# Kernel optimization log

Hardware: AMD Instinct MI355X
Metric: run time of the kernel (lower is better)

Reference implementation:

```python
import jax, jax.numpy as jnp
import numpy as np

N = 50000
E = 400000
NF = 320
HID = 320
EPS = 1e-08


def _linear(x, W, b=None):
    y = x @ W.T
    return y if b is None else y + b


def setup_inputs() -> dict:
    key = jax.random.key(0)
    ks = jax.random.split(key, 16)
    s = 0.05
    inp = {
        "h": jax.random.normal(ks[0], (N, NF), jnp.float32),
        "coord": jax.random.normal(ks[1], (N, 3), jnp.float32),
        "edge_index": jax.random.randint(ks[2], (2, E), 0, N, jnp.int32),
        # edge_mlp: Linear(2*NF+1 -> HID), SiLU, Linear(HID -> HID), SiLU
        "W_e1": jax.random.normal(ks[3], (HID, 2 * NF + 1), jnp.float32) * s,
        "b_e1": jnp.zeros((HID,), jnp.float32),
        "W_e2": jax.random.normal(ks[4], (HID, HID), jnp.float32) * s,
        "b_e2": jnp.zeros((HID,), jnp.float32),
        # node_mlp: Linear(HID+NF -> HID), SiLU, Linear(HID -> NF)
        "W_n1": jax.random.normal(ks[5], (HID, HID + NF), jnp.float32) * s,
        "b_n1": jnp.zeros((HID,), jnp.float32),
        "W_n2": jax.random.normal(ks[6], (NF, HID), jnp.float32) * s,
        "b_n2": jnp.zeros((NF,), jnp.float32),
        # coord_mlp: Linear(HID -> HID), SiLU, Linear(HID -> 1, no bias, xavier gain .001)
        "W_c1": jax.random.normal(ks[7], (HID, HID), jnp.float32) * s,
        "b_c1": jnp.zeros((HID,), jnp.float32),
        "W_c2": jax.random.normal(ks[8], (1, HID), jnp.float32) * 0.001,
    }
    return inp


def reference(h, coord, edge_index, W_e1, b_e1, W_e2, b_e2,
              W_n1, b_n1, W_n2, b_n2, W_c1, b_c1, W_c2):
    row, col = edge_index[0], edge_index[1]

    # coord2radial (normalize=True hard-coded in the module)
    coord_diff = coord[row] - coord[col]                      # [E,3]
    radial = jnp.sum(coord_diff ** 2, axis=1, keepdims=True)  # [E,1]
    norm = jax.lax.stop_gradient(jnp.sqrt(radial)) + EPS
    coord_diff = coord_diff / norm

    # edge model: gather endpoint feats, MLP with SiLU
    edge_in = jnp.concatenate([h[row], h[col], radial], axis=1)   # [E, 2*NF+1]
    m = jax.nn.silu(_linear(edge_in, W_e1, b_e1))
    m = jax.nn.silu(_linear(m, W_e2, b_e2))                       # [E, HID]

    # coord model: per-edge scalar weight, scatter-sum to nodes
    w = _linear(jax.nn.silu(_linear(m, W_c1, b_c1)), W_c2)        # [E,1]
    trans = coord_diff * w                                        # [E,3]
    coord_agg = jax.ops.segment_sum(trans, row, num_segments=N)   # [N,3]
    coord_out = coord + coord_agg

    # node model: scatter-sum messages, MLP, residual
    agg = jax.ops.segment_sum(m, row, num_segments=N)             # [N,HID]
    node_in = jnp.concatenate([h, agg], axis=1)                   # [N,HID+NF]
    out = _linear(jax.nn.silu(_linear(node_in, W_n1, b_n1)), W_n2, b_n2)
    h_out = h + out

    return (h_out, coord_out)
```

## Files before the change

### kernel.cpp

```cpp
#include <hip/hip_runtime.h>

#define NN 50000
#define NE 400000
#define NFD 320
#define NB1 196

typedef short bf16x8 __attribute__((ext_vector_type(8)));
typedef float f32x4 __attribute__((ext_vector_type(4)));

#define MFMA16 __builtin_amdgcn_mfma_f32_16x16x32_bf16

__device__ __forceinline__ unsigned short f2bf(float f){
  unsigned int u = __float_as_uint(f);
  u += 0x7fffu + ((u >> 16) & 1u);
  return (unsigned short)(u >> 16);
}
__device__ __forceinline__ unsigned int cvt_pk_bf16(float lo, float hi){
  unsigned int r;
  asm("v_cvt_pk_bf16_f32 %0, %1, %2" : "=v"(r) : "v"(lo), "v"(hi));
  return r;
}
__device__ __forceinline__ float bflo(unsigned int q){ return __uint_as_float(q << 16); }
__device__ __forceinline__ float bfhi(unsigned int q){ return __uint_as_float(q & 0xffff0000u); }
__device__ __forceinline__ float rcp_fast(float x){
  float r;
  asm("v_rcp_f32 %0, %1" : "=v"(r) : "v"(x));
  return r;
}
__device__ __forceinline__ float silu_f(float x){
  return x * rcp_fast(1.f + __expf(-x));
}

__device__ __forceinline__ void pack_w_body(const float* __restrict__ W,
                                            unsigned short* __restrict__ P,
                                            int kstride, int KS, int idx){
  if (idx >= 20 * KS * 64) return;
  int lane = idx & 63;
  int t  = idx >> 6;
  int ks = t % KS;
  int ct = t / KS;
  const float* src = W + (size_t)(ct*16 + (lane & 15)) * kstride + ks*32 + 8*(lane >> 4);
  unsigned int q[4];
  #pragma unroll
  for (int j = 0; j < 4; j++) q[j] = cvt_pk_bf16(src[2*j], src[2*j+1]);
  *(uint4*)(P + (size_t)idx * 8) = make_uint4(q[0], q[1], q[2], q[3]);
}

__device__ __forceinline__ void pack_stack_body(const float* __restrict__ We1,
                                                unsigned short* __restrict__ P, int idx){
  if (idx >= 40 * 10 * 64) return;
  int lane = idx & 63;
  int t  = idx >> 6;
  int ks = t % 10;
  int ct = t / 10;
  int o  = ct*16 + (lane & 15);
  int k  = ks*32 + 8*(lane >> 4);
  const float* src = (o < 320) ? (We1 + (size_t)o * 641 + k)
                               : (We1 + (size_t)(o - 320) * 641 + 320 + k);
  unsigned int q[4];
  #pragma unroll
  for (int j = 0; j < 4; j++) q[j] = cvt_pk_bf16(src[2*j], src[2*j+1]);
  *(uint4*)(P + (size_t)idx * 8) = make_uint4(q[0], q[1], q[2], q[3]);
}

#define PREP_PACK_B 176
#define PREP_CIN_B  293
#define PREP_HIST_B 782
__global__ void __launch_bounds__(512)
prep_k(const float* __restrict__ We2, const float* __restrict__ Wc1,
       const float* __restrict__ Wn1, const float* __restrict__ Wn2,
       const float* __restrict__ We1,
       unsigned short* __restrict__ We2p, unsigned short* __restrict__ Wc1p,
       unsigned short* __restrict__ Wn1p, unsigned short* __restrict__ Wn2p,
       unsigned short* __restrict__ Wsp, float* __restrict__ we1l,
       const float* __restrict__ coord, float* __restrict__ outc,
       const int* __restrict__ ei, int* __restrict__ cnt){
  int b = blockIdx.x;
  int tid = threadIdx.x;
  if (b < PREP_PACK_B){
    int idx = b*512 + tid;
    if (idx < 12800)       pack_w_body(We2, We2p, 320, 10, idx);
    else if (idx < 25600)  pack_w_body(Wc1, Wc1p, 320, 10, idx - 12800);
    else if (idx < 51200)  pack_w_body(Wn1, Wn1p, 640, 20, idx - 25600);
    else if (idx < 64000)  pack_w_body(Wn2, Wn2p, 320, 10, idx - 51200);
    else if (idx < 89600)  pack_stack_body(We1, Wsp, idx - 64000);
    else if (idx < 89920){
      int o = idx - 89600;
      we1l[o] = We1[(size_t)o * 641 + 640];
    }
  } else if (b < PREP_PACK_B + PREP_CIN_B){
    int i = (b - PREP_PACK_B)*512 + tid;
    if (i < NN*3) outc[i] = coord[i];
  } else {
    int e = (b - PREP_PACK_B - PREP_CIN_B)*512 + tid;
    if (e < NE) atomicAdd(&cnt[ei[e]], 1);
  }
}

__global__ void scan1(const int* __restrict__ cnt, int* __restrict__ cur,
                      int* __restrict__ bsum){
  __shared__ int sh[256];
  int tid = threadIdx.x;
  int i = blockIdx.x * 256 + tid;
  int v = (i < NN) ? cnt[i] : 0;
  sh[tid] = v;
  __syncthreads();
  for (int d = 1; d < 256; d <<= 1){
    int u = (tid >= d) ? sh[tid - d] : 0;
    __syncthreads();
    sh[tid] += u;
    __syncthreads();
  }
  if (i < NN) cur[i] = sh[tid] - v;
  if (tid == 255) bsum[blockIdx.x] = sh[255];
}

__global__ void scan2(int* __restrict__ bsum){
  __shared__ int sh[256];
  int tid = threadIdx.x;
  int v = (tid < NB1) ? bsum[tid] : 0;
  sh[tid] = v;
  __syncthreads();
  for (int d = 1; d < 256; d <<= 1){
    int u = (tid >= d) ? sh[tid - d] : 0;
    __syncthreads();
    sh[tid] += u;
    __syncthreads();
  }
  if (tid < NB1) bsum[tid] = sh[tid] - v;
}

__global__ void scan3(int* __restrict__ cur, const int* __restrict__ bsum){
  int i = blockIdx.x * 256 + threadIdx.x;
  if (i < NN) cur[i] += bsum[blockIdx.x];
}

__device__ __forceinline__ void gemm5(const unsigned short* __restrict__ s,
                                      const unsigned short* __restrict__ wp,
                                      int arow0, int arow1, int kl,
                                      int fragbase, int KST, int lane, f32x4 (&acc)[2][5]){
  const unsigned short* wl0 = wp + (size_t)fragbase * 512 + (size_t)lane * 8;
  bf16x8 b0[5], b1[5];
  #pragma unroll
  for (int t = 0; t < 5; t++) b0[t] = *(const bf16x8*)(wl0 + (t*KST + 0)*512);
  #pragma unroll
  for (int t = 0; t < 5; t++) b1[t] = *(const bf16x8*)(wl0 + (t*KST + 1)*512);
  #pragma unroll
  for (int ks = 0; ks < 10; ks++){
    bf16x8 a0 = *(const bf16x8*)(s + arow0*328 + ks*32 + kl);
    bf16x8 a1 = *(const bf16x8*)(s + arow1*328 + ks*32 + kl);
    bf16x8 cur[5];
    #pragma unroll
    for (int t = 0; t < 5; t++) cur[t] = (ks & 1) ? b1[t] : b0[t];
    if (ks < 8){
      #pragma unroll
      for (int t = 0; t < 5; t++){
        bf16x8 nv = *(const bf16x8*)(wl0 + (t*KST + ks + 2)*512);
        if (ks & 1) b1[t] = nv; else b0[t] = nv;
      }
    }
    #pragma unroll
    for (int t = 0; t < 5; t++){
      acc[0][t] = MFMA16(a0, cur[t], acc[0][t], 0, 0, 0);
      acc[1][t] = MFMA16(a1, cur[t], acc[1][t], 0, 0, 0);
    }
  }
}

#define SP_SCAT_B 782
__global__ void __launch_bounds__(512, 4)
scat_pre(const int* __restrict__ ei, int* __restrict__ cur, int* __restrict__ perm,
         const float* __restrict__ h, const unsigned short* __restrict__ Wsp,
         const float* __restrict__ be1, unsigned short* __restrict__ P){
  if (blockIdx.x < SP_SCAT_B){
    int e = blockIdx.x * 512 + threadIdx.x;
    if (e < NE){
      int p = atomicAdd(&cur[ei[e]], 1);
      perm[p] = e;
    }
    return;
  }
  __shared__ __align__(16) unsigned short s_h[32*328];

  const int tid  = threadIdx.x;
  const int lane = tid & 63;
  const int ch   = tid >> 6;
  const int n0   = (blockIdx.x - SP_SCAT_B) * 32;

  const int arow0 = (lane & 15);
  const int arow1 = 16 + (lane & 15);
  const int kl = 8 * (lane >> 4);
  const int rb = (lane >> 4) * 4;

  #pragma unroll
  for (int i = 0; i < 5; i++){
    int idx = tid + i*512;
    int r = idx / 80;
    int c = idx - r*80;
    int node = n0 + r;
    float4 v = (node < NN) ? *(const float4*)(h + (size_t)node*NFD + c*4)
                           : make_float4(0,0,0,0);
    *(uint2*)(s_h + r*328 + c*4) = make_uint2(cvt_pk_bf16(v.x, v.y), cvt_pk_bf16(v.z, v.w));
  }
  __syncthreads();

  f32x4 acc[2][5];
  #pragma unroll
  for (int rt = 0; rt < 2; rt++)
    #pragma unroll
    for (int t = 0; t < 5; t++) acc[rt][t] = {0.f,0.f,0.f,0.f};

  gemm5(s_h, Wsp, arow0, arow1, kl, ch*50, 10, lane, acc);

  #pragma unroll
  for (int rt = 0; rt < 2; rt++){
    #pragma unroll
    for (int t = 0; t < 5; t++){
      int o = (ch*5 + t)*16 + (lane & 15);
      float bb = (o < 320) ? be1[o] : 0.f;
      #pragma unroll
      for (int r = 0; r < 4; r++){
        int node = n0 + rt*16 + rb + r;
        if (node < NN) P[(size_t)node*640 + o] = f2bf(acc[rt][t][r] + bb);
      }
    }
  }
}

__global__ void __launch_bounds__(512, 4)
edge_kernel(const unsigned short* __restrict__ Pbf, const float* __restrict__ coord,
            const int* __restrict__ ei, const int* __restrict__ perm,
            const float* __restrict__ we1l,
            const unsigned short* __restrict__ We2p, const float* __restrict__ be2,
            const unsigned short* __restrict__ Wc1p, const float* __restrict__ bc1,
            const float* __restrict__ Wc2,
            unsigned short* __restrict__ agg, float* __restrict__ cacc)
{
  __shared__ __align__(16) unsigned short s_b[64*328];
  __shared__ float4 s_cd[64];
  __shared__ int s_row[64];
  __shared__ int s_col[64];
  __shared__ float s_w[64];

  const int tid  = threadIdx.x;
  const int lane = tid & 63;
  const int wv   = tid >> 6;
  const int ch   = wv & 3;
  const int rh   = wv >> 2;
  const int e0   = blockIdx.x * 64;

  if (tid < 64){
    int e = perm[e0 + tid];
    int r = ei[e];
    int c = ei[NE + e];
    s_row[tid] = r; s_col[tid] = c;
    s_w[tid] = 0.f;
    float dx = coord[r*3+0] - coord[c*3+0];
    float dy = coord[r*3+1] - coord[c*3+1];
    float dz = coord[r*3+2] - coord[c*3+2];
    float rad = dx*dx + dy*dy + dz*dz;
    float inv = 1.f / (sqrtf(rad) + 1e-8f);
    s_cd[tid] = make_float4(dx*inv, dy*inv, dz*inv, rad);
  }
  __syncthreads();

  const int arow0 = rh*32 + (lane & 15);
  const int arow1 = rh*32 + 16 + (lane & 15);
  const int kl = 8 * (lane >> 4);
  const int rb = (lane >> 4) * 4;

  {
    uint4 PR[5], PC[5];
    #pragma unroll
    for (int i = 0; i < 5; i++){
      int idx = tid + i*512;
      int r = idx / 40;
      int c = idx - r*40;
      PR[i] = *(const uint4*)(Pbf + (size_t)s_row[r]*640 + c*8);
      PC[i] = *(const uint4*)(Pbf + (size_t)s_col[r]*640 + 320 + c*8);
    }
    #pragma unroll
    for (int i = 0; i < 5; i++){
      int idx = tid + i*512;
      int r = idx / 40;
      int c = idx - r*40;
      uint4 pr = PR[i];
      uint4 pc = PC[i];
      float4 wA = *(const float4*)(we1l + c*8);
      float4 wB = *(const float4*)(we1l + c*8 + 4);
      float rad = s_cd[r].w;
      float v0 = silu_f(bflo(pr.x) + bflo(pc.x) + rad*wA.x);
      float v1 = silu_f(bfhi(pr.x) + bfhi(pc.x) + rad*wA.y);
      float v2 = silu_f(bflo(pr.y) + bflo(pc.y) + rad*wA.z);
      float v3 = silu_f(bfhi(pr.y) + bfhi(pc.y) + rad*wA.w);
      float v4 = silu_f(bflo(pr.z) + bflo(pc.z) + rad*wB.x);
      float v5 = silu_f(bfhi(pr.z) + bfhi(pc.z) + rad*wB.y);
      float v6 = silu_f(bflo(pr.w) + bflo(pc.w) + rad*wB.z);
      float v7 = silu_f(bfhi(pr.w) + bfhi(pc.w) + rad*wB.w);
      uint4 q;
      q.x = cvt_pk_bf16(v0, v1);
      q.y = cvt_pk_bf16(v2, v3);
      q.z = cvt_pk_bf16(v4, v5);
      q.w = cvt_pk_bf16(v6, v7);
      *(uint4*)(s_b + r*328 + c*8) = q;
    }
  }
  __syncthreads();

  f32x4 acc[2][5];

  #pragma unroll
  for (int rt = 0; rt < 2; rt++)
    #pragma unroll
    for (int t = 0; t < 5; t++) acc[rt][t] = {0.f,0.f,0.f,0.f};
  gemm5(s_b, We2p, arow0, arow1, kl, ch*50, 10, lane, acc);
  __syncthreads();
  #pragma unroll
  for (int t = 0; t < 5; t++){
    int o = (ch*5 + t)*16 + (lane & 15);
    float bb = be2[o];
    #pragma unroll
    for (int r = 0; r < 4; r++){
      float v0 = silu_f(acc[0][t][r] + bb);
      float v1 = silu_f(acc[1][t][r] + bb);
      unsigned int q = cvt_pk_bf16(v0, v1);
      int er = rh*32 + rb + r;
      s_b[er*328 + o] = (unsigned short)q;
      s_b[(er+16)*328 + o] = (unsigned short)(q >> 16);
    }
  }
  __syncthreads();

  #pragma unroll
  for (int rt = 0; rt < 2; rt++)
    #pragma unroll
    for (int t = 0; t < 5; t++) acc[rt][t] = {0.f,0.f,0.f,0.f};
  gemm5(s_b, Wc1p, arow0, arow1, kl, ch*50, 10, lane, acc);
  {
    float part[2][4];
    #pragma unroll
    for (int rt = 0; rt < 2; rt++)
      #pragma unroll
      for (int r = 0; r < 4; r++) part[rt][r] = 0.f;
    #pragma unroll
    for (int t = 0; t < 5; t++){
      int o = (ch*5 + t)*16 + (lane & 15);
      float bb = bc1[o];
      float wc = Wc2[o];
      #pragma unroll
      for (int rt = 0; rt < 2; rt++)
        #pragma unroll
        for (int r = 0; r < 4; r++)
          part[rt][r] = fmaf(silu_f(acc[rt][t][r] + bb), wc, part[rt][r]);
    }
    #pragma unroll
    for (int rt = 0; rt < 2; rt++)
      #pragma unroll
      for (int r = 0; r < 4; r++){
        float p = part[rt][r];
        p += __shfl_xor(p, 1);
        p += __shfl_xor(p, 2);
        p += __shfl_xor(p, 4);
        p += __shfl_xor(p, 8);
        if ((lane & 15) == 0)
          atomicAdd(&s_w[rh*32 + rt*16 + rb + r], p);
      }
  }
  __syncthreads();

  if (tid < 320){
    int seg = tid / 160;
    int p = tid - seg*160;
    float a0 = 0.f, a1 = 0.f;
    #pragma unroll
    for (int k = 0; k < 32; k++){
      int e = seg*32 + k;
      unsigned int q = *(const unsigned int*)(s_b + e*328 + p*2);
      a0 += bflo(q); a1 += bfhi(q);
      if (k == 31 || s_row[e+1] != s_row[e]){
        unsigned int val = cvt_pk_bf16(a0, a1);
        unsigned short* dst = agg + (size_t)s_row[e]*NFD + p*2;
        asm volatile("global_atomic_pk_add_bf16 %0, %1, off" :: "v"(dst), "v"(val) : "memory");
        a0 = 0.f; a1 = 0.f;
      }
    }
  }
  if (tid >= 384 && tid < 390){
    int idx = tid - 384;
    int seg = idx / 3;
    int d = idx - seg*3;
    float a = 0.f;
    #pragma unroll
    for (int k = 0; k < 32; k++){
      int e = seg*32 + k;
      float cdc = (d == 0) ? s_cd[e].x : (d == 1) ? s_cd[e].y : s_cd[e].z;
      a += cdc * s_w[e];
      if (k == 31 || s_row[e+1] != s_row[e]){
        atomicAdd(cacc + (size_t)s_row[e]*3 + d, a);
        a = 0.f;
      }
    }
  }
}

__global__ void __launch_bounds__(512, 4)
node_kernel(const float* __restrict__ h, const unsigned short* __restrict__ agg,
            const unsigned short* __restrict__ Wn1p, const float* __restrict__ bn1,
            const unsigned short* __restrict__ Wn2p, const float* __restrict__ bn2,
            float* __restrict__ hout)
{
  __shared__ __align__(16) unsigned short s_b[64*328];

  const int tid  = threadIdx.x;
  const int lane = tid & 63;
  const int wv   = tid >> 6;
  const int ch   = wv & 3;
  const int rh   = wv >> 2;
  const int n0   = blockIdx.x * 64;

  const int arow0 = rh*32 + (lane & 15);
  const int arow1 = rh*32 + 16 + (lane & 15);
  const int kl = 8 * (lane >> 4);
  const int rb = (lane >> 4) * 4;

  f32x4 acc[2][5];
  #pragma unroll
  for (int rt = 0; rt < 2; rt++)
    #pragma unroll
    for (int t = 0; t < 5; t++) acc[rt][t] = {0.f,0.f,0.f,0.f};

  #pragma unroll
  for (int i = 0; i < 10; i++){
    int idx = tid + i*512;
    int r = idx / 80;
    int c = idx - r*80;
    int node = n0 + r;
    float4 v = (node < NN) ? *(const float4*)(h + (size_t)node*NFD + c*4)
                           : make_float4(0,0,0,0);
    *(uint2*)(s_b + r*328 + c*4) = make_uint2(cvt_pk_bf16(v.x, v.y), cvt_pk_bf16(v.z, v.w));
  }
  __syncthreads();

  gemm5(s_b, Wn1p, arow0, arow1, kl, ch*100, 20, lane, acc);
  __syncthreads();

  #pragma unroll
  for (int i = 0; i < 5; i++){
    int idx = tid + i*512;
    int r = idx / 40;
    int c = idx - r*40;
    int node = n0 + r;
    uint4 v = (node < NN) ? *(const uint4*)(agg + (size_t)node*NFD + c*8)
                          : make_uint4(0,0,0,0);
    *(uint4*)(s_b + r*328 + c*8) = v;
  }
  __syncthreads();

  gemm5(s_b, Wn1p, arow0, arow1, kl, ch*100 + 10, 20, lane, acc);
  __syncthreads();

  #pragma unroll
  for (int t = 0; t < 5; t++){
    int o = (ch*5 + t)*16 + (lane & 15);
    float bb = bn1[o];
    #pragma unroll
    for (int r = 0; r < 4; r++){
      float v0 = silu_f(acc[0][t][r] + bb);
      float v1 = silu_f(acc[1][t][r] + bb);
      unsigned int q = cvt_pk_bf16(v0, v1);
      int er = rh*32 + rb + r;
      s_b[er*328 + o] = (unsigned short)q;
      s_b[(er+16)*328 + o] = (unsigned short)(q >> 16);
    }
  }
  __syncthreads();

  #pragma unroll
  for (int rt = 0; rt < 2; rt++)
    #pragma unroll
    for (int t = 0; t < 5; t++) acc[rt][t] = {0.f,0.f,0.f,0.f};
  gemm5(s_b, Wn2p, arow0, arow1, kl, ch*50, 10, lane, acc);
  #pragma unroll
  for (int t = 0; t < 5; t++){
    int o = (ch*5 + t)*16 + (lane & 15);
    float bb = bn2[o];
    #pragma unroll
    for (int r = 0; r < 4; r++){
      int node0 = n0 + rh*32 + rb + r;
      int node1 = node0 + 16;
      if (node0 < NN)
        hout[(size_t)node0*NFD + o] = h[(size_t)node0*NFD + o] + acc[0][t][r] + bb;
      if (node1 < NN)
        hout[(size_t)node1*NFD + o] = h[(size_t)node1*NFD + o] + acc[1][t][r] + bb;
    }
  }
}

extern "C" void kernel_launch(void* const* d_in, const int* in_sizes, int n_in,
                              void* d_out, int out_size, void* d_ws, size_t ws_size,
                              hipStream_t stream){
  const float* h     = (const float*)d_in[0];
  const float* coord = (const float*)d_in[1];
  const int*   ei    = (const int*)d_in[2];
  const float* We1 = (const float*)d_in[3];
  const float* be1 = (const float*)d_in[4];
  const float* We2 = (const float*)d_in[5];
  const float* be2 = (const float*)d_in[6];
  const float* Wn1 = (const float*)d_in[7];
  const float* bn1 = (const float*)d_in[8];
  const float* Wn2 = (const float*)d_in[9];
  const float* bn2 = (const float*)d_in[10];
  const float* Wc1 = (const float*)d_in[11];
  const float* bc1 = (const float*)d_in[12];
  const float* Wc2 = (const float*)d_in[13];

  char* ws = (char*)d_ws;
  unsigned short* We2p = (unsigned short*)(ws);
  unsigned short* Wc1p = (unsigned short*)(ws + 204800);
  unsigned short* Wn1p = (unsigned short*)(ws + 409600);
  unsigned short* Wn2p = (unsigned short*)(ws + 819200);
  unsigned short* Wsp  = (unsigned short*)(ws + 1024000);
  float*          we1l = (float*)(ws + 1433600);
  unsigned short* agg  = (unsigned short*)(ws + 1434880);
  int*            cnt  = (int*)(ws + 33434880);
  int*            cur  = (int*)(ws + 33634880);
  int*            perm = (int*)(ws + 33834880);
  int*            bsum = (int*)(ws + 35434880);

  float* hout = (float*)d_out;
  float* cout = hout + (size_t)NN * NFD;
  unsigned short* Pbf = (unsigned short*)d_out;

  hipMemsetAsync(agg, 0, (size_t)NN * NFD * 2, stream);
  hipMemsetAsync(cnt, 0, (size_t)NN * 4, stream);

  prep_k<<<PREP_PACK_B + PREP_CIN_B + PREP_HIST_B, 512, 0, stream>>>(
      We2, Wc1, Wn1, Wn2, We1, We2p, Wc1p, Wn1p, Wn2p, Wsp, we1l,
      coord, cout, ei, cnt);

  scan1<<<NB1, 256, 0, stream>>>(cnt, cur, bsum);
  scan2<<<1, 256, 0, stream>>>(bsum);
  scan3<<<NB1, 256, 0, stream>>>(cur, bsum);

  scat_pre<<<SP_SCAT_B + (NN + 31)/32, 512, 0, stream>>>(
      ei, cur, perm, h, Wsp, be1, Pbf);

  edge_kernel<<<NE/64, 512, 0, stream>>>(Pbf, coord, ei, perm, we1l,
                                         We2p, be2, Wc1p, bc1, Wc2, agg, cout);
  node_kernel<<<(NN + 63)/64, 512, 0, stream>>>(h, agg, Wn1p, bn1, Wn2p, bn2, hout);
}
```

Before: 550.6 us.

## Halve edge workgroup size and swizzle block IDs for XCD locality

After: 533.7 us (median of 2 runs). 3.1% less time.

```diff
diff --git a/kernel.cpp b/kernel.cpp
--- a/kernel.cpp
+++ b/kernel.cpp
@@ -227,7 +227,10 @@
   }
 }
 
-__global__ void __launch_bounds__(512, 4)
+#define EDGE_NWG (NE/32)
+#define SWZ_Q (EDGE_NWG/8)
+#define SWZ_R (EDGE_NWG%8)
+__global__ void __launch_bounds__(256, 5)
 edge_kernel(const unsigned short* __restrict__ Pbf, const float* __restrict__ coord,
             const int* __restrict__ ei, const int* __restrict__ perm,
             const float* __restrict__ we1l,
@@ -236,20 +239,23 @@
             const float* __restrict__ Wc2,
             unsigned short* __restrict__ agg, float* __restrict__ cacc)
 {
-  __shared__ __align__(16) unsigned short s_b[64*328];
-  __shared__ float4 s_cd[64];
-  __shared__ int s_row[64];
-  __shared__ int s_col[64];
-  __shared__ float s_w[64];
+  __shared__ __align__(16) unsigned short s_b[32*328];
+  __shared__ float4 s_cd[32];
+  __shared__ int s_row[32];
+  __shared__ int s_col[32];
+  __shared__ float s_w[32];
 
   const int tid  = threadIdx.x;
   const int lane = tid & 63;
-  const int wv   = tid >> 6;
-  const int ch   = wv & 3;
-  const int rh   = wv >> 2;
-  const int e0   = blockIdx.x * 64;
-
-  if (tid < 64){
+  const int ch   = tid >> 6;
+
+  const int orig = blockIdx.x;
+  const int xcd  = orig & 7;
+  const int k    = orig >> 3;
+  const int wgid = (xcd < SWZ_R ? xcd*(SWZ_Q+1) : SWZ_R*(SWZ_Q+1) + (xcd-SWZ_R)*SWZ_Q) + k;
+  const int e0   = wgid * 32;
+
+  if (tid < 32){
     int e = perm[e0 + tid];
     int r = ei[e];
     int c = ei[NE + e];
@@ -264,46 +270,35 @@
   }
   __syncthreads();
 
-  const int arow0 = rh*32 + (lane & 15);
-  const int arow1 = rh*32 + 16 + (lane & 15);
+  const int arow0 = (lane & 15);
+  const int arow1 = 16 + (lane & 15);
   const int kl = 8 * (lane >> 4);
   const int rb = (lane >> 4) * 4;
 
-  {
-    uint4 PR[5], PC[5];
-    #pragma unroll
-    for (int i = 0; i < 5; i++){
-      int idx = tid + i*512;
-      int r = idx / 40;
-      int c = idx - r*40;
-      PR[i] = *(const uint4*)(Pbf + (size_t)s_row[r]*640 + c*8);
-      PC[i] = *(const uint4*)(Pbf + (size_t)s_col[r]*640 + 320 + c*8);
-    }
-    #pragma unroll
-    for (int i = 0; i < 5; i++){
-      int idx = tid + i*512;
-      int r = idx / 40;
-      int c = idx - r*40;
-      uint4 pr = PR[i];
-      uint4 pc = PC[i];
-      float4 wA = *(const float4*)(we1l + c*8);
-      float4 wB = *(const float4*)(we1l + c*8 + 4);
-      float rad = s_cd[r].w;
-      float v0 = silu_f(bflo(pr.x) + bflo(pc.x) + rad*wA.x);
-      float v1 = silu_f(bfhi(pr.x) + bfhi(pc.x) + rad*wA.y);
-      float v2 = silu_f(bflo(pr.y) + bflo(pc.y) + rad*wA.z);
-      float v3 = silu_f(bfhi(pr.y) + bfhi(pc.y) + rad*wA.w);
-      float v4 = silu_f(bflo(pr.z) + bflo(pc.z) + rad*wB.x);
-      float v5 = silu_f(bfhi(pr.z) + bfhi(pc.z) + rad*wB.y);
-      float v6 = silu_f(bflo(pr.w) + bflo(pc.w) + rad*wB.z);
-      float v7 = silu_f(bfhi(pr.w) + bfhi(pc.w) + rad*wB.w);
-      uint4 q;
-      q.x = cvt_pk_bf16(v0, v1);
-      q.y = cvt_pk_bf16(v2, v3);
-      q.z = cvt_pk_bf16(v4, v5);
-      q.w = cvt_pk_bf16(v6, v7);
-      *(uint4*)(s_b + r*328 + c*8) = q;
-    }
+  #pragma unroll
+  for (int i = 0; i < 5; i++){
+    int idx = tid + i*256;
+    int r = idx / 40;
+    int c = idx - r*40;
+    uint4 pr = *(const uint4*)(Pbf + (size_t)s_row[r]*640 + c*8);
+    uint4 pc = *(const uint4*)(Pbf + (size_t)s_col[r]*640 + 320 + c*8);
+    float4 wA = *(const float4*)(we1l + c*8);
+    float4 wB = *(const float4*)(we1l + c*8 + 4);
+    float rad = s_cd[r].w;
+    float v0 = silu_f(bflo(pr.x) + bflo(pc.x) + rad*wA.x);
+    float v1 = silu_f(bfhi(pr.x) + bfhi(pc.x) + rad*wA.y);
+    float v2 = silu_f(bflo(pr.y) + bflo(pc.y) + rad*wA.z);
+    float v3 = silu_f(bfhi(pr.y) + bfhi(pc.y) + rad*wA.w);
+    float v4 = silu_f(bflo(pr.z) + bflo(pc.z) + rad*wB.x);
+    float v5 = silu_f(bfhi(pr.z) + bfhi(pc.z) + rad*wB.y);
+    float v6 = silu_f(bflo(pr.w) + bflo(pc.w) + rad*wB.z);
+    float v7 = silu_f(bfhi(pr.w) + bfhi(pc.w) + rad*wB.w);
+    uint4 q;
+    q.x = cvt_pk_bf16(v0, v1);
+    q.y = cvt_pk_bf16(v2, v3);
+    q.z = cvt_pk_bf16(v4, v5);
+    q.w = cvt_pk_bf16(v6, v7);
+    *(uint4*)(s_b + r*328 + c*8) = q;
   }
   __syncthreads();
 
@@ -324,7 +319,7 @@
       float v0 = silu_f(acc[0][t][r] + bb);
       float v1 = silu_f(acc[1][t][r] + bb);
       unsigned int q = cvt_pk_bf16(v0, v1);
-      int er = rh*32 + rb + r;
+      int er = rb + r;
       s_b[er*328 + o] = (unsigned short)q;
       s_b[(er+16)*328 + o] = (unsigned short)(q >> 16);
     }
@@ -363,21 +358,19 @@
         p += __shfl_xor(p, 4);
         p += __shfl_xor(p, 8);
         if ((lane & 15) == 0)
-          atomicAdd(&s_w[rh*32 + rt*16 + rb + r], p);
+          atomicAdd(&s_w[rt*16 + (lane >> 4)*4 + r], p);
       }
   }
   __syncthreads();
 
-  if (tid < 320){
-    int seg = tid / 160;
-    int p = tid - seg*160;
+  if (tid < 160){
+    int p = tid;
     float a0 = 0.f, a1 = 0.f;
     #pragma unroll
-    for (int k = 0; k < 32; k++){
-      int e = seg*32 + k;
+    for (int e = 0; e < 32; e++){
       unsigned int q = *(const unsigned int*)(s_b + e*328 + p*2);
       a0 += bflo(q); a1 += bfhi(q);
-      if (k == 31 || s_row[e+1] != s_row[e]){
+      if (e == 31 || s_row[e+1] != s_row[e]){
         unsigned int val = cvt_pk_bf16(a0, a1);
         unsigned short* dst = agg + (size_t)s_row[e]*NFD + p*2;
         asm volatile("global_atomic_pk_add_bf16 %0, %1, off" :: "v"(dst), "v"(val) : "memory");
@@ -385,17 +378,14 @@
       }
     }
   }
-  if (tid >= 384 && tid < 390){
-    int idx = tid - 384;
-    int seg = idx / 3;
-    int d = idx - seg*3;
+  if (tid >= 192 && tid < 195){
+    int d = tid - 192;
     float a = 0.f;
     #pragma unroll
-    for (int k = 0; k < 32; k++){
-      int e = seg*32 + k;
+    for (int e = 0; e < 32; e++){
       float cdc = (d == 0) ? s_cd[e].x : (d == 1) ? s_cd[e].y : s_cd[e].z;
       a += cdc * s_w[e];
-      if (k == 31 || s_row[e+1] != s_row[e]){
+      if (e == 31 || s_row[e+1] != s_row[e]){
         atomicAdd(cacc + (size_t)s_row[e]*3 + d, a);
         a = 0.f;
       }
@@ -545,7 +535,7 @@
   scat_pre<<<SP_SCAT_B + (NN + 31)/32, 512, 0, stream>>>(
       ei, cur, perm, h, Wsp, be1, Pbf);
 
-  edge_kernel<<<NE/64, 512, 0, stream>>>(Pbf, coord, ei, perm, we1l,
-                                         We2p, be2, Wc1p, bc1, Wc2, agg, cout);
+  edge_kernel<<<EDGE_NWG, 256, 0, stream>>>(Pbf, coord, ei, perm, we1l,
+                                            We2p, be2, Wc1p, bc1, Wc2, agg, cout);
   node_kernel<<<(NN + 63)/64, 512, 0, stream>>>(h, agg, Wn1p, bn1, Wn2p, bn2, hout);
 }
```
